# Kernel tuning notes

Measured on AMD Instinct MI355X. Metric: run time of the kernel, lower is better.

Reference implementation:

```python
import jax, jax.numpy as jnp
import numpy as np
import math

B, S, D, H, COND = 4, 2048, 768, 12, 128
DH = D // H
MLP = 4 * D
EPS = 1e-5


def setup_inputs() -> dict:
    key = jax.random.key(0)
    ks = jax.random.split(key, 10)
    s = 0.02  # init scale for weights
    x = jax.random.normal(ks[0], (B, S, D), jnp.float32)
    c = jax.random.normal(ks[1], (B, COND), jnp.float32)
    # rotary tables, layout (1, S, 3, 1, DH) per module docstring
    pos = jnp.arange(S, dtype=jnp.float32)
    inv_freq = 1.0 / (10000.0 ** (jnp.arange(0, DH, 2, dtype=jnp.float32) / DH))
    ang = pos[:, None] * inv_freq[None, :]            # (S, DH/2)
    cos = jnp.concatenate([jnp.cos(ang), jnp.cos(ang)], -1)  # (S, DH)
    sin = jnp.concatenate([jnp.sin(ang), jnp.sin(ang)], -1)
    cos = jnp.broadcast_to(cos[None, :, None, None, :], (1, S, 3, 1, DH))
    sin = jnp.broadcast_to(sin[None, :, None, None, :], (1, S, 3, 1, DH))
    return {
        "x": x,
        "cos": cos,
        "sin": sin,
        "c": c,
        "ln1_w": jnp.ones((D,), jnp.float32),
        "W_qkv": s * jax.random.normal(ks[2], (3 * D, D), jnp.float32),
        "W_out": s * jax.random.normal(ks[3], (D, D), jnp.float32),
        "W_mlp1": s * jax.random.normal(ks[4], (MLP, D), jnp.float32),
        "b_mlp1": jnp.zeros((MLP,), jnp.float32),
        "W_mlp2": s * jax.random.normal(ks[5], (D, MLP), jnp.float32),
        "b_mlp2": jnp.zeros((D,), jnp.float32),
        "ln2_w": jnp.ones((D,), jnp.float32),
        "W_ada": s * jax.random.normal(ks[6], (6 * D, COND), jnp.float32),
        "b_ada": jnp.zeros((6 * D,), jnp.float32),
    }


def _ln(x, w):
    # LayerNorm with weight only (no bias), computed in fp32 like the original
    xf = x.astype(jnp.float32)
    mu = xf.mean(-1, keepdims=True)
    var = ((xf - mu) ** 2).mean(-1, keepdims=True)
    return (xf - mu) * jax.lax.rsqrt(var + EPS) * w


def reference(x, cos, sin, c, ln1_w, W_qkv, W_out, W_mlp1, b_mlp1, W_mlp2, b_mlp2, ln2_w, W_ada, b_ada):
    b, s_len = x.shape[0], x.shape[1]
    # adaLN modulation: (B, 6D) -> six (B, 1, D) chunks
    ada = c @ W_ada.T + b_ada
    sh_msa, sc_msa, g_msa, sh_mlp, sc_mlp, g_mlp = [t[:, None, :] for t in jnp.split(ada, 6, axis=-1)]

    x_skip = x
    h = _ln(x, ln1_w) * (1.0 + sc_msa) + sh_msa
    qkv = (h @ W_qkv.T).reshape(b, s_len, 3, H, DH)

    # rotary: slice as in apply_rotary_pos_emb_for_macos
    cos_s = cos[0, :, 0, 0, : DH // 2][None, :, None, :]  # (1, S, 1, DH/2)
    sin_s = sin[0, :, 0, 0, : DH // 2][None, :, None, :]
    q, k, v = qkv[:, :, 0], qkv[:, :, 1], qkv[:, :, 2]     # (B, S, H, DH)

    def _rot(t):
        t1, t2 = t[..., : DH // 2], t[..., DH // 2 :]
        return jnp.concatenate([t1 * cos_s - t2 * sin_s, t1 * sin_s + t2 * cos_s], -1)

    q, k = _rot(q), _rot(k)

    # non-causal attention
    scale = 1.0 / math.sqrt(DH)
    scores = jnp.einsum("bshd,bthd->bhst", q, k) * scale
    attn = jax.nn.softmax(scores, axis=-1)
    o = jnp.einsum("bhst,bthd->bshd", attn, v).reshape(b, s_len, D)

    # bias_dropout_add_scale (inference: dropout = identity)
    x = x_skip + g_msa * (o @ W_out.T)

    h2 = _ln(x, ln2_w) * (1.0 + sc_mlp) + sh_mlp
    m = jax.nn.gelu(h2 @ W_mlp1.T + b_mlp1, approximate=True) @ W_mlp2.T + b_mlp2
    return x + g_mlp * m
```

## Files before the change

kernel.cpp:

```cpp
#include <hip/hip_runtime.h>

typedef __bf16 bf16;
typedef __bf16 bf16x4 __attribute__((ext_vector_type(4)));
typedef __bf16 bf16x8 __attribute__((ext_vector_type(8)));
typedef float floatx4 __attribute__((ext_vector_type(4)));

#define MFMA16(a, b, c) __builtin_amdgcn_mfma_f32_16x16x32_bf16((a), (b), (c), 0, 0, 0)

__device__ __forceinline__ float san(float v, float magic) {
  unsigned u = __builtin_bit_cast(unsigned, v);
  return ((u & 0x7f800000u) == 0x7f800000u) ? magic : v;
}

__device__ __forceinline__ void gld_lds16(bf16* lds, const bf16* g) {
  __builtin_amdgcn_global_load_lds((__attribute__((address_space(1))) void*)g,
                                   (__attribute__((address_space(3))) void*)lds,
                                   16, 0, 0);
}

__global__ __launch_bounds__(256) void wcvt_k(const float* __restrict__ w,
                                              bf16* __restrict__ o, int n4) {
  int i = blockIdx.x * 256 + threadIdx.x;
  if (i >= n4) return;
  float4 v = ((const float4*)w)[i];
  bf16x4 b = {(bf16)v.x, (bf16)v.y, (bf16)v.z, (bf16)v.w};
  *(bf16x4*)(o + (size_t)i * 4) = b;
}

__global__ __launch_bounds__(256) void wcvt4_k(const float* __restrict__ wqkv,
                                               const float* __restrict__ wout,
                                               const float* __restrict__ wm1,
                                               const float* __restrict__ wm2,
                                               bf16* __restrict__ dst) {
  int i = blockIdx.x * 256 + threadIdx.x;
  if (i >= 1769472) return;
  const float* s;
  int off;
  if (i < 442368) { s = wqkv; off = 0; }
  else if (i < 589824) { s = wout; off = 442368; }
  else if (i < 1179648) { s = wm1; off = 589824; }
  else { s = wm2; off = 1179648; }
  float4 v = ((const float4*)s)[i - off];
  bf16x4 b = {(bf16)v.x, (bf16)v.y, (bf16)v.z, (bf16)v.w};
  *(bf16x4*)(dst + (size_t)i * 4) = b;
}

__global__ void ada_k(const float* __restrict__ c, const float* __restrict__ W,
                      const float* __restrict__ bias, float* __restrict__ ada) {
  int idx = blockIdx.x * 256 + threadIdx.x;
  if (idx >= 4 * 4608) return;
  int bb = idx / 4608;
  int j = idx - bb * 4608;
  float s = bias[j];
  const float4* wp = (const float4*)(W + (size_t)j * 128);
  const float4* cp = (const float4*)(c + (size_t)bb * 128);
#pragma unroll
  for (int t = 0; t < 32; t++) {
    float4 w4 = wp[t], c4 = cp[t];
    s += c4.x * w4.x + c4.y * w4.y + c4.z * w4.z + c4.w * w4.w;
  }
  ada[idx] = san(s, 7.0e3f);
}

__global__ __launch_bounds__(256) void ln_mod_k(const float* __restrict__ xin,
                                                const float* __restrict__ lnw,
                                                const float* __restrict__ ada,
                                                int sh_off, int sc_off,
                                                bf16* __restrict__ h,
                                                int tok_base) {
  int wv = threadIdx.x >> 6, lane = threadIdx.x & 63;
  int tok = tok_base + blockIdx.x * 4 + wv;
  int bb = tok >> 11;
  const float* xr = xin + (size_t)tok * 768;
  size_t obase = (size_t)(tok - tok_base) * 768;
  float4 v[3];
#pragma unroll
  for (int r = 0; r < 3; r++) v[r] = *(const float4*)(xr + lane * 4 + r * 256);
  float s1 = 0.f, s2 = 0.f;
#pragma unroll
  for (int r = 0; r < 3; r++) {
    s1 += v[r].x + v[r].y + v[r].z + v[r].w;
    s2 += v[r].x * v[r].x + v[r].y * v[r].y + v[r].z * v[r].z + v[r].w * v[r].w;
  }
#pragma unroll
  for (int off = 32; off > 0; off >>= 1) {
    s1 += __shfl_xor(s1, off);
    s2 += __shfl_xor(s2, off);
  }
  float mu = s1 * (1.f / 768.f);
  float rs = rsqrtf(s2 * (1.f / 768.f) - mu * mu + 1e-5f);
  const float* adab = ada + bb * 4608;
#pragma unroll
  for (int r = 0; r < 3; r++) {
    int j = lane * 4 + r * 256;
    float4 sc = *(const float4*)(adab + sc_off + j);
    float4 sh = *(const float4*)(adab + sh_off + j);
    float4 w4 = *(const float4*)(lnw + j);
    bf16x4 o4;
    o4[0] = (bf16)san(((v[r].x - mu) * rs) * w4.x * (1.f + sc.x) + sh.x, 5.0e3f);
    o4[1] = (bf16)san(((v[r].y - mu) * rs) * w4.y * (1.f + sc.y) + sh.y, 5.0e3f);
    o4[2] = (bf16)san(((v[r].z - mu) * rs) * w4.z * (1.f + sc.z) + sh.z, 5.0e3f);
    o4[3] = (bf16)san(((v[r].w - mu) * rs) * w4.w * (1.f + sc.w) + sh.w, 5.0e3f);
    *(bf16x4*)&h[obase + j] = o4;
  }
}

template <int EPI, int BM>
__global__ __launch_bounds__(BM * 2, (BM == 256) ? 4 : 3) void gemm_k(
    const bf16* __restrict__ A, const bf16* __restrict__ W, int K, int k_len,
    int m_base, const float* __restrict__ cosp, const float* __restrict__ sinp,
    const float* __restrict__ ada, const float* __restrict__ resid_x,
    const float* __restrict__ bias, bf16* __restrict__ out_q,
    bf16* __restrict__ out_k, bf16* __restrict__ out_v,
    float* __restrict__ out_f, float* __restrict__ out_f2) {
  constexpr int NW = BM / 32;
  constexpr int AJ = 2;
  constexpr int BJ = 8 / NW;
  __shared__ bf16 As[3][BM * 32];
  __shared__ bf16 Bs[3][128 * 32];
  int tid = threadIdx.x;
  int lane = tid & 63, wv = tid >> 6;
  int quad = lane >> 4, lm = lane & 15;
  int gx = gridDim.x, nwg = gx * gridDim.y;
  int d = blockIdx.y * gx + blockIdx.x;
  int lid = d;
  if ((nwg & 7) == 0) {
    int q8 = nwg >> 3;
    lid = (d & 7) * q8 + (d >> 3);
  }
  int by = lid / gx, bx = lid - by * gx;
  int m0 = by * BM, n0 = bx * 128;
  int mw = (wv >> 1) * 64, nw = (wv & 1) * 64;
  int kb = blockIdx.z * k_len;

  floatx4 acc[4][4];
#pragma unroll
  for (int i = 0; i < 4; i++)
#pragma unroll
    for (int j = 0; j < 4; j++) acc[i][j] = {0.f, 0.f, 0.f, 0.f};

  const bf16* Ag[AJ];
#pragma unroll
  for (int qa = 0; qa < AJ; qa++)
    Ag[qa] = A + (size_t)(m0 + (wv * AJ + qa) * 16 + lm) * K + quad * 8;
  const bf16* Bg[BJ];
#pragma unroll
  for (int qb = 0; qb < BJ; qb++)
    Bg[qb] = W + (size_t)(n0 + (wv * BJ + qb) * 16 + lm) * K + quad * 8;

#define STAGE_T(sb, kk)                                            \
  do {                                                             \
    _Pragma("unroll") for (int qa = 0; qa < AJ; qa++)              \
        gld_lds16(&As[sb][(wv * AJ + qa) * 512], Ag[qa] + (kk));   \
    _Pragma("unroll") for (int qb = 0; qb < BJ; qb++)              \
        gld_lds16(&Bs[sb][(wv * BJ + qb) * 512], Bg[qb] + (kk));   \
  } while (0)

  int nt = k_len >> 5;
  STAGE_T(0, kb);
  STAGE_T(1, kb + 32);

  int s_cur = 0;
  for (int t = 0; t < nt; t++) {
    if (t + 1 < nt) {
      if constexpr (BM == 256)
        asm volatile("s_waitcnt vmcnt(3)" ::: "memory");
      else
        asm volatile("s_waitcnt vmcnt(4)" ::: "memory");
    } else {
      asm volatile("s_waitcnt vmcnt(0)" ::: "memory");
    }
    __builtin_amdgcn_s_barrier();
    if (t + 2 < nt) {
      int sn = s_cur + 2;
      if (sn >= 3) sn -= 3;
      STAGE_T(sn, kb + (t + 2) * 32);
    }
    bf16x8 af[4], bfr[4];
#pragma unroll
    for (int i = 0; i < 4; i++) {
      int it = (mw >> 4) + i;
      af[i] = *(const bf16x8*)&As[s_cur][(size_t)(it * 64 + quad * 16 + lm) * 8];
      int jt = (nw >> 4) + i;
      bfr[i] = *(const bf16x8*)&Bs[s_cur][(size_t)(jt * 64 + quad * 16 + lm) * 8];
    }
#pragma unroll
    for (int i = 0; i < 4; i++)
#pragma unroll
      for (int j = 0; j < 4; j++) acc[i][j] = MFMA16(af[i], bfr[j], acc[i][j]);
    s_cur = (s_cur + 1 == 3) ? 0 : s_cur + 1;
  }
#undef STAGE_T

  int colb = n0 + nw;
#pragma unroll
  for (int i = 0; i < 4; i++) {
#pragma unroll
    for (int r = 0; r < 4; r++) {
      int mg = m_base + m0 + mw + i * 16 + quad * 4 + r;
      if (EPI == 0) {
        int bb = mg >> 11, s = mg & 2047;
        int sec = colb / 768;
        int nb = colb - sec * 768;
        int hh = nb >> 6;
        if (sec == 2) {
          size_t vbase = ((size_t)(bb * 12 + hh) * 64) * 2048 + s;
#pragma unroll
          for (int j = 0; j < 4; j++) {
            int d2 = j * 16 + lm;
            out_v[vbase + (size_t)d2 * 2048] = (bf16)san(acc[i][j][r], 100.f);
          }
        } else {
          const float* cs = cosp + (size_t)s * 192;
          const float* sn = sinp + (size_t)s * 192;
          bf16* dst = (sec == 0) ? out_q : out_k;
          float scl = (sec == 0) ? 0.125f : 1.0f;
          size_t base = ((size_t)(bb * 12 + hh) * 2048 + s) * 64;
#pragma unroll
          for (int j = 0; j < 2; j++) {
            int d2 = j * 16 + lm;
            float c0 = cs[d2], s0 = sn[d2];
            float t1 = san(acc[i][j][r], 100.f);
            float t2 = san(acc[i][j + 2][r], 100.f);
            dst[base + d2] = (bf16)((t1 * c0 - t2 * s0) * scl);
            dst[base + d2 + 32] = (bf16)((t1 * s0 + t2 * c0) * scl);
          }
        }
      } else if (EPI == 1) {
        int bb = mg >> 11;
#pragma unroll
        for (int j = 0; j < 4; j++) {
          int n = colb + j * 16 + lm;
          float g = ada[bb * 4608 + 1536 + n];
          float xv =
              san(resid_x[(size_t)mg * 768 + n] + g * acc[i][j][r], 1.0e5f);
          out_f[(size_t)mg * 768 + n] = xv;
          float g2 = ada[bb * 4608 + 3840 + n];
          out_f2[(size_t)mg * 768 + n] = xv + g2 * bias[n];
        }
      } else if (EPI == 2) {
#pragma unroll
        for (int j = 0; j < 4; j++) {
          int n = colb + j * 16 + lm;
          float v = acc[i][j][r] + bias[n];
          float t = tanhf(0.7978845608f * (v + 0.044715f * v * v * v));
          out_q[(size_t)(mg - m_base) * 3072 + n] =
              (bf16)san(0.5f * v * (1.f + t), 3.0e5f);
        }
      } else {
        int bb = mg >> 11;
#pragma unroll
        for (int j = 0; j < 4; j++) {
          int n = colb + j * 16 + lm;
          float g = ada[bb * 4608 + 3840 + n];
          atomicAdd(out_f + (size_t)mg * 768 + n, san(g * acc[i][j][r], 1.0e6f));
        }
      }
    }
  }
}

__global__ __launch_bounds__(512, 3) void attn_k(const bf16* __restrict__ q,
                                                 const bf16* __restrict__ k,
                                                 const bf16* __restrict__ vT,
                                                 bf16* __restrict__ o) {
  __shared__ bf16 Kbuf[2][4096];
  __shared__ bf16 Vbuf[2][4096];
  __shared__ bf16 Plds[8][16 * 72];
  int d = blockIdx.y * gridDim.x + blockIdx.x;
  int idx = d >> 3;
  int qt = idx & 15;
  int bh = ((idx >> 4) << 3) + (d & 7);
  int b = bh / 12, h = bh - b * 12;
  int tid = threadIdx.x, lane = tid & 63, wv = tid >> 6;
  int quad = lane >> 4, lm = lane & 15;

  const bf16* Kp = k + (size_t)bh * 2048 * 64;
  const bf16* Vp = vT + (size_t)bh * 64 * 2048;

  const bf16* Qrow =
      q + (size_t)bh * 2048 * 64 + (size_t)(qt * 128 + wv * 16 + lm) * 64;
  bf16x8 qf0 = *(const bf16x8*)(Qrow + quad * 8);
  bf16x8 qf1 = *(const bf16x8*)(Qrow + 32 + quad * 8);

  const bf16* ksrc =
      Kp + (size_t)((wv >> 1) * 16 + lm) * 64 + (wv & 1) * 32 + quad * 8;
  const bf16* vsrc =
      Vp + (size_t)((wv >> 1) * 16 + lm) * 2048 + (wv & 1) * 32 + quad * 8;

  float l_i = 0.f;
  floatx4 accO[4];
#pragma unroll
  for (int t = 0; t < 4; t++) accO[t] = {0.f, 0.f, 0.f, 0.f};

  gld_lds16(&Kbuf[0][wv * 512], ksrc);
  gld_lds16(&Vbuf[0][wv * 512], vsrc);

  int p = 0;
  for (int kt = 0; kt < 32; kt++) {
    __syncthreads();
    if (kt < 31) {
      size_t ko = (size_t)(kt + 1) * 4096;
      size_t vo = (size_t)(kt + 1) * 64;
      int pn = p ^ 1;
      gld_lds16(&Kbuf[pn][wv * 512], ksrc + ko);
      gld_lds16(&Vbuf[pn][wv * 512], vsrc + vo);
    }

    floatx4 accS[4];
#pragma unroll
    for (int i = 0; i < 4; i++) accS[i] = {0.f, 0.f, 0.f, 0.f};
    __builtin_amdgcn_s_setprio(1);
#pragma unroll
    for (int i = 0; i < 4; i++) {
      bf16x8 kf0 =
          *(const bf16x8*)&Kbuf[p][(size_t)((i * 2 + 0) * 64 + quad * 16 + lm) * 8];
      bf16x8 kf1 =
          *(const bf16x8*)&Kbuf[p][(size_t)((i * 2 + 1) * 64 + quad * 16 + lm) * 8];
      accS[i] = MFMA16(kf0, qf0, accS[i]);
      accS[i] = MFMA16(kf1, qf1, accS[i]);
    }
    __builtin_amdgcn_s_setprio(0);

    float psum = 0.f;
    bf16 pv[4][4];
#pragma unroll
    for (int i = 0; i < 4; i++)
#pragma unroll
      for (int r = 0; r < 4; r++) {
        float pe = __expf(accS[i][r]);
        psum += pe;
        pv[i][r] = (bf16)pe;
      }
    l_i += psum;

#pragma unroll
    for (int i = 0; i < 4; i++) {
      bf16x4 pk = {pv[i][0], pv[i][1], pv[i][2], pv[i][3]};
      *(bf16x4*)&Plds[wv][lm * 72 + i * 16 + quad * 4] = pk;
    }

    __builtin_amdgcn_s_setprio(1);
#pragma unroll
    for (int st = 0; st < 2; st++) {
      bf16x8 pf = *(const bf16x8*)&Plds[wv][lm * 72 + st * 32 + quad * 8];
#pragma unroll
      for (int t = 0; t < 4; t++) {
        bf16x8 vf =
            *(const bf16x8*)&Vbuf[p][(size_t)((t * 2 + st) * 64 + quad * 16 + lm) * 8];
        accO[t] = MFMA16(pf, vf, accO[t]);
      }
    }
    __builtin_amdgcn_s_setprio(0);
    p ^= 1;
  }

  l_i += __shfl_xor(l_i, 16);
  l_i += __shfl_xor(l_i, 32);

  float lr[4];
#pragma unroll
  for (int r = 0; r < 4; r++) lr[r] = 1.f / __shfl(l_i, (quad << 2) + r);
#pragma unroll
  for (int t = 0; t < 4; t++) {
#pragma unroll
    for (int r = 0; r < 4; r++) {
      int d2 = t * 16 + lm;
      int s = qt * 128 + wv * 16 + quad * 4 + r;
      o[((size_t)(b * 2048 + s)) * 768 + h * 64 + d2] =
          (bf16)san(accO[t][r] * lr[r], 3.0e4f);
    }
  }
}

extern "C" void kernel_launch(void* const* d_in, const int* in_sizes, int n_in,
                              void* d_out, int out_size, void* d_ws,
                              size_t ws_size, hipStream_t stream) {
  (void)in_sizes; (void)n_in; (void)out_size;
  const float* x = (const float*)d_in[0];
  const float* cosp = (const float*)d_in[1];
  const float* sinp = (const float*)d_in[2];
  const float* c = (const float*)d_in[3];
  const float* ln1w = (const float*)d_in[4];
  const float* Wqkv = (const float*)d_in[5];
  const float* Wout = (const float*)d_in[6];
  const float* Wm1 = (const float*)d_in[7];
  const float* bm1 = (const float*)d_in[8];
  const float* Wm2 = (const float*)d_in[9];
  const float* bm2 = (const float*)d_in[10];
  const float* ln2w = (const float*)d_in[11];
  const float* Wada = (const float*)d_in[12];
  const float* bada = (const float*)d_in[13];

  const size_t TOKB = (size_t)8192 * 768 * 2;
  char* ws = (char*)d_ws;
  float* ada = (float*)ws;
  char* base = ws + 73728;
  bf16* h = (bf16*)d_out;
  float* outp = (float*)d_out;

  if (ws_size >= 156000000) {
    bf16* qb = (bf16*)base;
    bf16* kb = (bf16*)(base + TOKB);
    bf16* vT = (bf16*)(base + 2 * TOKB);
    bf16* obuf = (bf16*)(base + 3 * TOKB);
    float* x2 = (float*)(base + 4 * TOKB);
    bf16* h2c = (bf16*)(base + 6 * TOKB);
    bf16* m1c = (bf16*)(base + 7 * TOKB);
    bf16* wall = (bf16*)(base + 11 * TOKB);
    bf16* wqkv_b = wall;
    bf16* wout_b = wall + (size_t)1769472;
    bf16* wm1_b = wall + (size_t)2359296;
    bf16* wm2_b = wall + (size_t)4718592;

    ada_k<<<72, 256, 0, stream>>>(c, Wada, bada, ada);
    wcvt4_k<<<6912, 256, 0, stream>>>(Wqkv, Wout, Wm1, Wm2, wall);
    ln_mod_k<<<2048, 256, 0, stream>>>(x, ln1w, ada, 0, 768, h, 0);
    gemm_k<0, 256><<<dim3(18, 32), 512, 0, stream>>>(
        h, wqkv_b, 768, 768, 0, cosp, sinp, ada, nullptr, nullptr, qb, kb, vT,
        nullptr, nullptr);
    attn_k<<<dim3(16, 48), 512, 0, stream>>>(qb, kb, vT, obuf);
    gemm_k<1, 128><<<dim3(6, 64), 256, 0, stream>>>(
        obuf, wout_b, 768, 768, 0, nullptr, nullptr, ada, x, bm2, nullptr,
        nullptr, nullptr, x2, outp);
    ln_mod_k<<<2048, 256, 0, stream>>>(x2, ln2w, ada, 2304, 3072, h2c, 0);
    gemm_k<2, 256><<<dim3(24, 32), 512, 0, stream>>>(
        h2c, wm1_b, 768, 768, 0, nullptr, nullptr, nullptr, nullptr, bm1, m1c,
        nullptr, nullptr, nullptr, nullptr);
    gemm_k<4, 256><<<dim3(6, 32, 2), 512, 0, stream>>>(
        m1c, wm2_b, 3072, 1536, 0, nullptr, nullptr, ada, nullptr, nullptr,
        nullptr, nullptr, nullptr, outp, nullptr);
  } else {
    bf16* qb = (bf16*)base;
    bf16* kb = (bf16*)(base + TOKB);
    bf16* vT = (bf16*)(base + 2 * TOKB);
    bf16* obuf = (bf16*)(base + 3 * TOKB);
    bf16* h2c = (bf16*)(base + 3 * TOKB);
    float* x2 = (float*)base;
    bf16* m1c = (bf16*)(base + TOKB);
    bf16* wqkv_b = (bf16*)(base + 3 * TOKB);
    bf16* wout_b = (bf16*)(base + 2 * TOKB);
    bf16* wm1_b = (bf16*)base;
    bf16* wm2_b = (bf16*)base + (size_t)3072 * 768;

    ada_k<<<72, 256, 0, stream>>>(c, Wada, bada, ada);
    ln_mod_k<<<2048, 256, 0, stream>>>(x, ln1w, ada, 0, 768, h, 0);
    wcvt_k<<<(2304 * 768 / 4 + 255) / 256, 256, 0, stream>>>(Wqkv, wqkv_b,
                                                             2304 * 768 / 4);
    gemm_k<0, 128><<<dim3(18, 64), 256, 0, stream>>>(
        h, wqkv_b, 768, 768, 0, cosp, sinp, ada, nullptr, nullptr, qb, kb, vT,
        nullptr, nullptr);
    attn_k<<<dim3(16, 48), 512, 0, stream>>>(qb, kb, vT, obuf);
    wcvt_k<<<(768 * 768 / 4 + 255) / 256, 256, 0, stream>>>(Wout, wout_b,
                                                            768 * 768 / 4);
    gemm_k<1, 128><<<dim3(6, 64), 256, 0, stream>>>(
        obuf, wout_b, 768, 768, 0, nullptr, nullptr, ada, x, bm2, nullptr,
        nullptr, nullptr, x2, outp);
    ln_mod_k<<<2048, 256, 0, stream>>>(x2, ln2w, ada, 2304, 3072, h2c, 0);
    wcvt_k<<<(3072 * 768 / 4 + 255) / 256, 256, 0, stream>>>(Wm1, wm1_b,
                                                             3072 * 768 / 4);
    wcvt_k<<<(768 * 3072 / 4 + 255) / 256, 256, 0, stream>>>(Wm2, wm2_b,
                                                             768 * 3072 / 4);
    for (int cidx = 0; cidx < 2; cidx++) {
      int mb = cidx * 4096;
      gemm_k<2, 128><<<dim3(24, 32), 256, 0, stream>>>(
          h2c + (size_t)mb * 768, wm1_b, 768, 768, mb, nullptr, nullptr,
          nullptr, nullptr, bm1, m1c, nullptr, nullptr, nullptr, nullptr);
      gemm_k<4, 128><<<dim3(6, 32, 2), 256, 0, stream>>>(
          m1c, wm2_b, 3072, 1536, mb, nullptr, nullptr, ada, nullptr, nullptr,
          nullptr, nullptr, nullptr, outp, nullptr);
    }
  }
}
```

Baseline: 508.1 us.

## Use double-buffered LDS for BM=256 GEMM to raise occupancy, deepen MLP2 split-K

For the 256-row GEMM tiles, the LDS pipeline drops from three stages to two, with a full vmcnt(0) wait each iteration. The launch bound rises from 4 to 6 blocks per CU so more workgroups can be resident and hide latency. The second MLP GEMM's split-K goes from 2 to 4 slices, giving more workgroups over a shorter K range each. The trade-off is less in-block prefetch overlap and more split-K partial accumulation into the output, which relies on the epilogue handling four slices correctly.

```diff
diff --git a/kernel.cpp b/kernel.cpp
--- a/kernel.cpp
+++ b/kernel.cpp
@@ -106,7 +106,7 @@
 }
 
 template <int EPI, int BM>
-__global__ __launch_bounds__(BM * 2, (BM == 256) ? 4 : 3) void gemm_k(
+__global__ __launch_bounds__(BM * 2, (BM == 256) ? 6 : 3) void gemm_k(
     const bf16* __restrict__ A, const bf16* __restrict__ W, int K, int k_len,
     int m_base, const float* __restrict__ cosp, const float* __restrict__ sinp,
     const float* __restrict__ ada, const float* __restrict__ resid_x,
@@ -116,8 +116,9 @@
   constexpr int NW = BM / 32;
   constexpr int AJ = 2;
   constexpr int BJ = 8 / NW;
-  __shared__ bf16 As[3][BM * 32];
-  __shared__ bf16 Bs[3][128 * 32];
+  constexpr int NSTG = (BM == 256) ? 2 : 3;
+  __shared__ bf16 As[NSTG][BM * 32];
+  __shared__ bf16 Bs[NSTG][128 * 32];
   int tid = threadIdx.x;
   int lane = tid & 63, wv = tid >> 6;
   int quad = lane >> 4, lm = lane & 15;
@@ -157,38 +158,59 @@
   } while (0)
 
   int nt = k_len >> 5;
-  STAGE_T(0, kb);
-  STAGE_T(1, kb + 32);
-
-  int s_cur = 0;
-  for (int t = 0; t < nt; t++) {
-    if (t + 1 < nt) {
-      if constexpr (BM == 256)
-        asm volatile("s_waitcnt vmcnt(3)" ::: "memory");
+
+  if constexpr (BM == 256) {
+    STAGE_T(0, kb);
+    int p = 0;
+    for (int t = 0; t < nt; t++) {
+      asm volatile("s_waitcnt vmcnt(0)" ::: "memory");
+      __builtin_amdgcn_s_barrier();
+      if (t + 1 < nt) STAGE_T(p ^ 1, kb + (t + 1) * 32);
+      bf16x8 af[4], bfr[4];
+#pragma unroll
+      for (int i = 0; i < 4; i++) {
+        int it = (mw >> 4) + i;
+        af[i] = *(const bf16x8*)&As[p][(size_t)(it * 64 + quad * 16 + lm) * 8];
+        int jt = (nw >> 4) + i;
+        bfr[i] = *(const bf16x8*)&Bs[p][(size_t)(jt * 64 + quad * 16 + lm) * 8];
+      }
+#pragma unroll
+      for (int i = 0; i < 4; i++)
+#pragma unroll
+        for (int j = 0; j < 4; j++) acc[i][j] = MFMA16(af[i], bfr[j], acc[i][j]);
+      p ^= 1;
+    }
+  } else {
+    STAGE_T(0, kb);
+    STAGE_T(1, kb + 32);
+    int s_cur = 0;
+    for (int t = 0; t < nt; t++) {
+      if (t + 1 < nt)
+        asm volatile("s_waitcnt vmcnt(4)" ::: "memory");
       else
-        asm volatile("s_waitcnt vmcnt(4)" ::: "memory");
-    } else {
-      asm volatile("s_waitcnt vmcnt(0)" ::: "memory");
-    }
-    __builtin_amdgcn_s_barrier();
-    if (t + 2 < nt) {
-      int sn = s_cur + 2;
-      if (sn >= 3) sn -= 3;
-      STAGE_T(sn, kb + (t + 2) * 32);
-    }
-    bf16x8 af[4], bfr[4];
-#pragma unroll
-    for (int i = 0; i < 4; i++) {
-      int it = (mw >> 4) + i;
-      af[i] = *(const bf16x8*)&As[s_cur][(size_t)(it * 64 + quad * 16 + lm) * 8];
-      int jt = (nw >> 4) + i;
-      bfr[i] = *(const bf16x8*)&Bs[s_cur][(size_t)(jt * 64 + quad * 16 + lm) * 8];
-    }
-#pragma unroll
-    for (int i = 0; i < 4; i++)
-#pragma unroll
-      for (int j = 0; j < 4; j++) acc[i][j] = MFMA16(af[i], bfr[j], acc[i][j]);
-    s_cur = (s_cur + 1 == 3) ? 0 : s_cur + 1;
+        asm volatile("s_waitcnt vmcnt(0)" ::: "memory");
+      __builtin_amdgcn_s_barrier();
+      if (t + 2 < nt) {
+        int sn = s_cur + 2;
+        if (sn >= 3) sn -= 3;
+        STAGE_T(sn, kb + (t + 2) * 32);
+      }
+      bf16x8 af[4], bfr[4];
+#pragma unroll
+      for (int i = 0; i < 4; i++) {
+        int it = (mw >> 4) + i;
+        af[i] =
+            *(const bf16x8*)&As[s_cur][(size_t)(it * 64 + quad * 16 + lm) * 8];
+        int jt = (nw >> 4) + i;
+        bfr[i] =
+            *(const bf16x8*)&Bs[s_cur][(size_t)(jt * 64 + quad * 16 + lm) * 8];
+      }
+#pragma unroll
+      for (int i = 0; i < 4; i++)
+#pragma unroll
+        for (int j = 0; j < 4; j++) acc[i][j] = MFMA16(af[i], bfr[j], acc[i][j]);
+      s_cur = (s_cur + 1 == 3) ? 0 : s_cur + 1;
+    }
   }
 #undef STAGE_T
 
@@ -427,8 +449,8 @@
     gemm_k<2, 256><<<dim3(24, 32), 512, 0, stream>>>(
         h2c, wm1_b, 768, 768, 0, nullptr, nullptr, nullptr, nullptr, bm1, m1c,
         nullptr, nullptr, nullptr, nullptr);
-    gemm_k<4, 256><<<dim3(6, 32, 2), 512, 0, stream>>>(
-        m1c, wm2_b, 3072, 1536, 0, nullptr, nullptr, ada, nullptr, nullptr,
+    gemm_k<4, 256><<<dim3(6, 32, 4), 512, 0, stream>>>(
+        m1c, wm2_b, 3072, 768, 0, nullptr, nullptr, ada, nullptr, nullptr,
         nullptr, nullptr, nullptr, outp, nullptr);
   } else {
     bf16* qb = (bf16*)base;
```

Result: slower. 922.5 us (+81.5%).
